# Kernel tuning notes

Hardware: AMD Instinct MI355X
Metric: run time of the kernel (lower is better)

The kernel has to match this reference:

```python
import jax, jax.numpy as jnp
import numpy as np


def setup_inputs() -> dict:
    key = jax.random.key(0)
    k1, k2, k3 = jax.random.split(key, 3)
    B, M, J = 4096, 64, 24  # batch, n_max_markers, n_joints
    points = jax.random.normal(k1, (B, M, 3), dtype=jnp.float32)
    weight = jax.random.uniform(k2, (B, M, J), dtype=jnp.float32)  # positive soft weights
    offset = jax.random.normal(k3, (B, M, J, 3), dtype=jnp.float32)
    return {"points": points, "weight": weight, "offset": offset}


def reference(points, weight, offset):
    # P: per-joint marker offsets (B, J, 3, M); Q: world marker positions (B, 1, 3, M)
    P = jnp.transpose(offset, (0, 2, 3, 1))
    Q = jnp.transpose(points, (0, 2, 1))[:, None]
    w = jnp.transpose(weight, (0, 2, 1))[:, :, None]  # (B, J, 1, M)

    wsum = jnp.sum(w, axis=-1)                   # (B, J, 1)
    P_ = jnp.sum(P * w, axis=-1) / wsum          # (B, J, 3) weighted centroid of offsets
    Q_ = jnp.sum(Q * w, axis=-1) / wsum          # (B, J, 3) weighted centroid of markers

    X = P - P_[..., None]                        # (B, J, 3, M)
    Y = Q - Q_[..., None]                        # (B, J, 3, M) via broadcast

    # Cross-covariance S = X @ Y^T (NOTE: original multiplies un-weighted centered coords)
    S = jnp.einsum('bjdm,bjem->bjde', X, Y)      # (B, J, 3, 3)

    U, _, Vh = jnp.linalg.svd(S)
    V = jnp.swapaxes(Vh, -1, -2)
    Ut = jnp.swapaxes(U, -1, -2)
    det = jnp.linalg.det(jnp.matmul(V, Ut))      # (B, J) reflection correction
    Ut = Ut.at[..., -1, :].multiply(det[..., None])
    R = jnp.matmul(V, Ut)                        # (B, J, 3, 3) optimal rotation
    t = Q_[..., None] - jnp.matmul(R, P_[..., None])  # (B, J, 3, 1)
    return R, t
```

## Files before the change

### kernel.cpp

```cpp
#include <hip/hip_runtime.h>


constexpr int M = 64;
constexpr int J = 24;
constexpr int NACC = 22;
constexpr int NWS  = 15;

constexpr int L4_W = 0;
constexpr int L4_O = 384;
constexpr int L4_P = 1536;
constexpr int L4_N = 1584;

template<int P, int Q>
__device__ __forceinline__ void jrot(float A[4][4], float V[4][4]) {
    float apq = A[P][Q];
    float theta = (A[Q][Q] - A[P][P]) * __builtin_amdgcn_rcpf(2.0f * apq);
    float t = __builtin_amdgcn_rcpf(fabsf(theta) + __builtin_amdgcn_sqrtf(fmaf(theta, theta, 1.0f)));
    t = (theta < 0.0f) ? -t : t;
    t = (apq == 0.0f) ? 0.0f : t;
    float c = __builtin_amdgcn_rsqf(fmaf(t, t, 1.0f));
    float s = t * c;
#pragma unroll
    for (int k = 0; k < 4; ++k) {
        float akp = A[k][P], akq = A[k][Q];
        A[k][P] = c * akp - s * akq;
        A[k][Q] = s * akp + c * akq;
    }
#pragma unroll
    for (int k = 0; k < 4; ++k) {
        float apk = A[P][k], aqk = A[Q][k];
        A[P][k] = c * apk - s * aqk;
        A[Q][k] = s * apk + c * aqk;
        float vkp = V[k][P], vkq = V[k][Q];
        V[k][P] = c * vkp - s * vkq;
        V[k][Q] = s * vkp + c * vkq;
    }
}

__device__ __forceinline__ void horn_solve(
    float S00, float S01, float S02, float S10, float S11, float S12,
    float S20, float S21, float S22,
    float cP0, float cP1, float cP2, float cQ0, float cQ1, float cQ2,
    float* __restrict__ Rout, float* __restrict__ tout)
{
    float A[4][4], V[4][4];
    A[0][0] = S00 + S11 + S22;
    A[0][1] = A[1][0] = S12 - S21;
    A[0][2] = A[2][0] = S20 - S02;
    A[0][3] = A[3][0] = S01 - S10;
    A[1][1] = S00 - S11 - S22;
    A[1][2] = A[2][1] = S01 + S10;
    A[1][3] = A[3][1] = S02 + S20;
    A[2][2] = -S00 + S11 - S22;
    A[2][3] = A[3][2] = S12 + S21;
    A[3][3] = -S00 - S11 + S22;
#pragma unroll
    for (int r = 0; r < 4; ++r)
#pragma unroll
        for (int c = 0; c < 4; ++c)
            V[r][c] = (r == c) ? 1.0f : 0.0f;

#pragma unroll 1
    for (int sweep = 0; sweep < 6; ++sweep) {
        jrot<0, 1>(A, V); jrot<0, 2>(A, V); jrot<0, 3>(A, V);
        jrot<1, 2>(A, V); jrot<1, 3>(A, V); jrot<2, 3>(A, V);
    }

    float best = A[0][0];
    float qw = V[0][0], qx = V[1][0], qy = V[2][0], qz = V[3][0];
#pragma unroll
    for (int i = 1; i < 4; ++i) {
        bool better = A[i][i] > best;
        best = better ? A[i][i] : best;
        qw = better ? V[0][i] : qw;
        qx = better ? V[1][i] : qx;
        qy = better ? V[2][i] : qy;
        qz = better ? V[3][i] : qz;
    }
    float nrm = __builtin_amdgcn_rsqf(qw * qw + qx * qx + qy * qy + qz * qz);
    qw *= nrm; qx *= nrm; qy *= nrm; qz *= nrm;

    float R00 = 1.f - 2.f * (qy * qy + qz * qz);
    float R01 = 2.f * (qx * qy - qw * qz);
    float R02 = 2.f * (qx * qz + qw * qy);
    float R10 = 2.f * (qx * qy + qw * qz);
    float R11 = 1.f - 2.f * (qx * qx + qz * qz);
    float R12 = 2.f * (qy * qz - qw * qx);
    float R20 = 2.f * (qx * qz - qw * qy);
    float R21 = 2.f * (qy * qz + qw * qx);
    float R22 = 1.f - 2.f * (qx * qx + qy * qy);

    Rout[0] = R00; Rout[1] = R01; Rout[2] = R02;
    Rout[3] = R10; Rout[4] = R11; Rout[5] = R12;
    Rout[6] = R20; Rout[7] = R21; Rout[8] = R22;
    tout[0] = cQ0 - (R00 * cP0 + R01 * cP1 + R02 * cP2);
    tout[1] = cQ1 - (R10 * cP0 + R11 * cP1 + R12 * cP2);
    tout[2] = cQ2 - (R20 * cP0 + R21 * cP1 + R22 * cP2);
}

__global__ __launch_bounds__(256, 4) void kabsch_fused(
    const float* __restrict__ points,
    const float* __restrict__ weight,
    const float* __restrict__ offset,
    float* __restrict__ out,
    int bj_total)
{
    const int b = blockIdx.x;
    const int t = threadIdx.x;

    __shared__ float4 lds4[L4_N];

    const float4* wb4 = (const float4*)(weight + (size_t)b * (M * J));
    const float4* ob4 = (const float4*)(offset + (size_t)b * (M * J * 3));
    const float4* pb4 = (const float4*)(points + (size_t)b * (M * 3));

    float4 o0_ = ob4[t];
    float4 o1_ = ob4[t + 256];
    float4 o2_ = ob4[t + 512];
    float4 o3_ = ob4[t + 768];
    float4 w0_ = wb4[t];
    float4 o4_ = {0.f, 0.f, 0.f, 0.f};
    float4 w1_ = {0.f, 0.f, 0.f, 0.f};
    float4 p0_ = {0.f, 0.f, 0.f, 0.f};
    if (t < 128) { o4_ = ob4[1024 + t]; w1_ = wb4[256 + t]; }
    if (t < 48)  { p0_ = pb4[t]; }

    lds4[L4_O + t]        = o0_;
    lds4[L4_O + 256 + t]  = o1_;
    lds4[L4_O + 512 + t]  = o2_;
    lds4[L4_O + 768 + t]  = o3_;
    lds4[L4_W + t]        = w0_;
    if (t < 128) { lds4[L4_O + 1024 + t] = o4_; lds4[L4_W + 256 + t] = w1_; }
    if (t < 48)  { lds4[L4_P + t] = p0_; }

    __syncthreads();

    const int lane = t & 63;
    const int wv   = t >> 6;
    const int kk   = lane & 7;
    const int jj   = (lane >> 3) + wv * 8;
    const bool prod = (jj < J);

    float acc[NACC];
#pragma unroll
    for (int n = 0; n < NACC; ++n) acc[n] = 0.0f;

    if (prod) {
        const float* w_s = (const float*)lds4;
        const float* o_s = (const float*)lds4 + 4 * L4_O;
        const float* p_s = (const float*)lds4 + 4 * L4_P;

#pragma unroll
        for (int i = 0; i < M / 8; ++i) {
            const int m = i * 8 + kk;
            float w  = w_s[m * J + jj];
            float o0 = o_s[m * 72 + jj * 3 + 0];
            float o1 = o_s[m * 72 + jj * 3 + 1];
            float o2 = o_s[m * 72 + jj * 3 + 2];
            float p0 = p_s[m * 3 + 0];
            float p1 = p_s[m * 3 + 1];
            float p2 = p_s[m * 3 + 2];
            acc[0] += w;
            acc[1] = fmaf(w, o0, acc[1]);  acc[2] = fmaf(w, o1, acc[2]);  acc[3] = fmaf(w, o2, acc[3]);
            acc[4] = fmaf(w, p0, acc[4]);  acc[5] = fmaf(w, p1, acc[5]);  acc[6] = fmaf(w, p2, acc[6]);
            acc[7] += o0; acc[8] += o1; acc[9] += o2;
            acc[10] += p0; acc[11] += p1; acc[12] += p2;
            acc[13] = fmaf(o0, p0, acc[13]); acc[14] = fmaf(o0, p1, acc[14]); acc[15] = fmaf(o0, p2, acc[15]);
            acc[16] = fmaf(o1, p0, acc[16]); acc[17] = fmaf(o1, p1, acc[17]); acc[18] = fmaf(o1, p2, acc[18]);
            acc[19] = fmaf(o2, p0, acc[19]); acc[20] = fmaf(o2, p1, acc[20]); acc[21] = fmaf(o2, p2, acc[21]);
        }

#pragma unroll
        for (int n = 0; n < NACC; ++n) {
            float v = acc[n];
            v += __shfl_xor(v, 1);
            v += __shfl_xor(v, 2);
            v += __shfl_xor(v, 4);
            acc[n] = v;
        }
    }

    __syncthreads();

    float* sv_s = (float*)lds4;
    if (prod && kk == 0) {
        const float inv = __builtin_amdgcn_rcpf(acc[0]);
        const float cP0 = acc[1] * inv, cP1 = acc[2] * inv, cP2 = acc[3] * inv;
        const float cQ0 = acc[4] * inv, cQ1 = acc[5] * inv, cQ2 = acc[6] * inv;
        const float To0 = acc[7], To1 = acc[8], To2 = acc[9];
        const float Tp0 = acc[10], Tp1 = acc[11], Tp2 = acc[12];
        const float fM = (float)M;
        float Sv[NWS];
        Sv[0] = acc[13] - cP0 * Tp0 - cQ0 * To0 + fM * cP0 * cQ0;
        Sv[1] = acc[14] - cP0 * Tp1 - cQ1 * To0 + fM * cP0 * cQ1;
        Sv[2] = acc[15] - cP0 * Tp2 - cQ2 * To0 + fM * cP0 * cQ2;
        Sv[3] = acc[16] - cP1 * Tp0 - cQ0 * To1 + fM * cP1 * cQ0;
        Sv[4] = acc[17] - cP1 * Tp1 - cQ1 * To1 + fM * cP1 * cQ1;
        Sv[5] = acc[18] - cP1 * Tp2 - cQ2 * To1 + fM * cP1 * cQ2;
        Sv[6] = acc[19] - cP2 * Tp0 - cQ0 * To2 + fM * cP2 * cQ0;
        Sv[7] = acc[20] - cP2 * Tp1 - cQ1 * To2 + fM * cP2 * cQ1;
        Sv[8] = acc[21] - cP2 * Tp2 - cQ2 * To2 + fM * cP2 * cQ2;
        Sv[9]  = cP0; Sv[10] = cP1; Sv[11] = cP2;
        Sv[12] = cQ0; Sv[13] = cQ1; Sv[14] = cQ2;
#pragma unroll
        for (int n = 0; n < NWS; ++n) sv_s[n * J + jj] = Sv[n];
    }

    __syncthreads();

    if (t < J) {
        float v[NWS];
#pragma unroll
        for (int n = 0; n < NWS; ++n) v[n] = sv_s[n * J + t];
        float Rr[9], tr[3];
        horn_solve(v[0], v[1], v[2], v[3], v[4], v[5], v[6], v[7], v[8],
                   v[9], v[10], v[11], v[12], v[13], v[14], Rr, tr);
        const int bj = b * J + t;
        float* Rout = out + (size_t)bj * 9;
#pragma unroll
        for (int n = 0; n < 9; ++n) Rout[n] = Rr[n];
        float* tout = out + (size_t)bj_total * 9 + (size_t)bj * 3;
        tout[0] = tr[0]; tout[1] = tr[1]; tout[2] = tr[2];
    }
}

extern "C" void kernel_launch(void* const* d_in, const int* in_sizes, int n_in,
                              void* d_out, int out_size, void* d_ws, size_t ws_size,
                              hipStream_t stream) {
    const float* points = (const float*)d_in[0];
    const float* weight = (const float*)d_in[1];
    const float* offset = (const float*)d_in[2];
    float* out = (float*)d_out;

    int B = in_sizes[0] / (M * 3);
    int bj_total = B * J;

    kabsch_fused<<<B, 256, 0, stream>>>(points, weight, offset, out, bj_total);
}
```

Measured before the change: 144.1 us.

## Process four batches per block with register-prefetched global loads

Each block now handles four batch items in sequence. It prefetches the next item's weight, offset and point data into registers while the current item is reduced out of LDS, so global-load latency overlaps with compute. The per-item results are staged in a dedicated LDS array, and a single Horn eigen-solve pass then uses 96 threads instead of 24. In exchange the grid is four times smaller (1024 blocks), which cuts parallelism, and the prefetch raises register pressure.

```diff
diff --git a/kernel.cpp b/kernel.cpp
--- a/kernel.cpp
+++ b/kernel.cpp
@@ -5,6 +5,7 @@
 constexpr int J = 24;
 constexpr int NACC = 22;
 constexpr int NWS  = 15;
+constexpr int BPG  = 4;
 
 constexpr int L4_W = 0;
 constexpr int L4_O = 384;
@@ -103,37 +104,13 @@
     const float* __restrict__ weight,
     const float* __restrict__ offset,
     float* __restrict__ out,
-    int bj_total)
+    int B, int bj_total)
 {
-    const int b = blockIdx.x;
-    const int t = threadIdx.x;
+    const int b0 = blockIdx.x * BPG;
+    const int t  = threadIdx.x;
 
     __shared__ float4 lds4[L4_N];
-
-    const float4* wb4 = (const float4*)(weight + (size_t)b * (M * J));
-    const float4* ob4 = (const float4*)(offset + (size_t)b * (M * J * 3));
-    const float4* pb4 = (const float4*)(points + (size_t)b * (M * 3));
-
-    float4 o0_ = ob4[t];
-    float4 o1_ = ob4[t + 256];
-    float4 o2_ = ob4[t + 512];
-    float4 o3_ = ob4[t + 768];
-    float4 w0_ = wb4[t];
-    float4 o4_ = {0.f, 0.f, 0.f, 0.f};
-    float4 w1_ = {0.f, 0.f, 0.f, 0.f};
-    float4 p0_ = {0.f, 0.f, 0.f, 0.f};
-    if (t < 128) { o4_ = ob4[1024 + t]; w1_ = wb4[256 + t]; }
-    if (t < 48)  { p0_ = pb4[t]; }
-
-    lds4[L4_O + t]        = o0_;
-    lds4[L4_O + 256 + t]  = o1_;
-    lds4[L4_O + 512 + t]  = o2_;
-    lds4[L4_O + 768 + t]  = o3_;
-    lds4[L4_W + t]        = w0_;
-    if (t < 128) { lds4[L4_O + 1024 + t] = o4_; lds4[L4_W + 256 + t] = w1_; }
-    if (t < 48)  { lds4[L4_P + t] = p0_; }
-
-    __syncthreads();
+    __shared__ float  sv_s[BPG][NWS][J + 1];
 
     const int lane = t & 63;
     const int wv   = t >> 6;
@@ -141,86 +118,117 @@
     const int jj   = (lane >> 3) + wv * 8;
     const bool prod = (jj < J);
 
-    float acc[NACC];
-#pragma unroll
-    for (int n = 0; n < NACC; ++n) acc[n] = 0.0f;
-
-    if (prod) {
-        const float* w_s = (const float*)lds4;
-        const float* o_s = (const float*)lds4 + 4 * L4_O;
-        const float* p_s = (const float*)lds4 + 4 * L4_P;
-
-#pragma unroll
-        for (int i = 0; i < M / 8; ++i) {
-            const int m = i * 8 + kk;
-            float w  = w_s[m * J + jj];
-            float o0 = o_s[m * 72 + jj * 3 + 0];
-            float o1 = o_s[m * 72 + jj * 3 + 1];
-            float o2 = o_s[m * 72 + jj * 3 + 2];
-            float p0 = p_s[m * 3 + 0];
-            float p1 = p_s[m * 3 + 1];
-            float p2 = p_s[m * 3 + 2];
-            acc[0] += w;
-            acc[1] = fmaf(w, o0, acc[1]);  acc[2] = fmaf(w, o1, acc[2]);  acc[3] = fmaf(w, o2, acc[3]);
-            acc[4] = fmaf(w, p0, acc[4]);  acc[5] = fmaf(w, p1, acc[5]);  acc[6] = fmaf(w, p2, acc[6]);
-            acc[7] += o0; acc[8] += o1; acc[9] += o2;
-            acc[10] += p0; acc[11] += p1; acc[12] += p2;
-            acc[13] = fmaf(o0, p0, acc[13]); acc[14] = fmaf(o0, p1, acc[14]); acc[15] = fmaf(o0, p2, acc[15]);
-            acc[16] = fmaf(o1, p0, acc[16]); acc[17] = fmaf(o1, p1, acc[17]); acc[18] = fmaf(o1, p2, acc[18]);
-            acc[19] = fmaf(o2, p0, acc[19]); acc[20] = fmaf(o2, p1, acc[20]); acc[21] = fmaf(o2, p2, acc[21]);
+    float4 r_o0, r_o1, r_o2, r_o3, r_o4, r_w0, r_w1, r_p0;
+    auto load_batch = [&](int bb) {
+        bb = bb < B ? bb : B - 1;
+        const float4* wb4 = (const float4*)(weight + (size_t)bb * (M * J));
+        const float4* ob4 = (const float4*)(offset + (size_t)bb * (M * J * 3));
+        const float4* pb4 = (const float4*)(points + (size_t)bb * (M * 3));
+        r_o0 = ob4[t];
+        r_o1 = ob4[t + 256];
+        r_o2 = ob4[t + 512];
+        r_o3 = ob4[t + 768];
+        r_w0 = wb4[t];
+        if (t < 128) { r_o4 = ob4[1024 + t]; r_w1 = wb4[256 + t]; }
+        if (t < 48)  { r_p0 = pb4[t]; }
+    };
+
+    load_batch(b0);
+
+#pragma unroll 1
+    for (int g = 0; g < BPG; ++g) {
+        lds4[L4_O + t]       = r_o0;
+        lds4[L4_O + 256 + t] = r_o1;
+        lds4[L4_O + 512 + t] = r_o2;
+        lds4[L4_O + 768 + t] = r_o3;
+        lds4[L4_W + t]       = r_w0;
+        if (t < 128) { lds4[L4_O + 1024 + t] = r_o4; lds4[L4_W + 256 + t] = r_w1; }
+        if (t < 48)  { lds4[L4_P + t] = r_p0; }
+
+        __syncthreads();
+
+        if (g + 1 < BPG) load_batch(b0 + g + 1);
+
+        float acc[NACC];
+#pragma unroll
+        for (int n = 0; n < NACC; ++n) acc[n] = 0.0f;
+
+        if (prod) {
+            const float* w_s = (const float*)lds4;
+            const float* o_s = (const float*)lds4 + 4 * L4_O;
+            const float* p_s = (const float*)lds4 + 4 * L4_P;
+
+#pragma unroll
+            for (int i = 0; i < M / 8; ++i) {
+                const int m = i * 8 + kk;
+                float w  = w_s[m * J + jj];
+                float o0 = o_s[m * 72 + jj * 3 + 0];
+                float o1 = o_s[m * 72 + jj * 3 + 1];
+                float o2 = o_s[m * 72 + jj * 3 + 2];
+                float p0 = p_s[m * 3 + 0];
+                float p1 = p_s[m * 3 + 1];
+                float p2 = p_s[m * 3 + 2];
+                acc[0] += w;
+                acc[1] = fmaf(w, o0, acc[1]);  acc[2] = fmaf(w, o1, acc[2]);  acc[3] = fmaf(w, o2, acc[3]);
+                acc[4] = fmaf(w, p0, acc[4]);  acc[5] = fmaf(w, p1, acc[5]);  acc[6] = fmaf(w, p2, acc[6]);
+                acc[7] += o0; acc[8] += o1; acc[9] += o2;
+                acc[10] += p0; acc[11] += p1; acc[12] += p2;
+                acc[13] = fmaf(o0, p0, acc[13]); acc[14] = fmaf(o0, p1, acc[14]); acc[15] = fmaf(o0, p2, acc[15]);
+                acc[16] = fmaf(o1, p0, acc[16]); acc[17] = fmaf(o1, p1, acc[17]); acc[18] = fmaf(o1, p2, acc[18]);
+                acc[19] = fmaf(o2, p0, acc[19]); acc[20] = fmaf(o2, p1, acc[20]); acc[21] = fmaf(o2, p2, acc[21]);
+            }
+
+#pragma unroll
+            for (int n = 0; n < NACC; ++n) {
+                float v = acc[n];
+                v += __shfl_xor(v, 1);
+                v += __shfl_xor(v, 2);
+                v += __shfl_xor(v, 4);
+                acc[n] = v;
+            }
+
+            if (kk == 0) {
+                const float inv = __builtin_amdgcn_rcpf(acc[0]);
+                const float cP0 = acc[1] * inv, cP1 = acc[2] * inv, cP2 = acc[3] * inv;
+                const float cQ0 = acc[4] * inv, cQ1 = acc[5] * inv, cQ2 = acc[6] * inv;
+                const float To0 = acc[7], To1 = acc[8], To2 = acc[9];
+                const float Tp0 = acc[10], Tp1 = acc[11], Tp2 = acc[12];
+                const float fM = (float)M;
+                sv_s[g][0][jj]  = acc[13] - cP0 * Tp0 - cQ0 * To0 + fM * cP0 * cQ0;
+                sv_s[g][1][jj]  = acc[14] - cP0 * Tp1 - cQ1 * To0 + fM * cP0 * cQ1;
+                sv_s[g][2][jj]  = acc[15] - cP0 * Tp2 - cQ2 * To0 + fM * cP0 * cQ2;
+                sv_s[g][3][jj]  = acc[16] - cP1 * Tp0 - cQ0 * To1 + fM * cP1 * cQ0;
+                sv_s[g][4][jj]  = acc[17] - cP1 * Tp1 - cQ1 * To1 + fM * cP1 * cQ1;
+                sv_s[g][5][jj]  = acc[18] - cP1 * Tp2 - cQ2 * To1 + fM * cP1 * cQ2;
+                sv_s[g][6][jj]  = acc[19] - cP2 * Tp0 - cQ0 * To2 + fM * cP2 * cQ0;
+                sv_s[g][7][jj]  = acc[20] - cP2 * Tp1 - cQ1 * To2 + fM * cP2 * cQ1;
+                sv_s[g][8][jj]  = acc[21] - cP2 * Tp2 - cQ2 * To2 + fM * cP2 * cQ2;
+                sv_s[g][9][jj]  = cP0; sv_s[g][10][jj] = cP1; sv_s[g][11][jj] = cP2;
+                sv_s[g][12][jj] = cQ0; sv_s[g][13][jj] = cQ1; sv_s[g][14][jj] = cQ2;
+            }
         }
 
-#pragma unroll
-        for (int n = 0; n < NACC; ++n) {
-            float v = acc[n];
-            v += __shfl_xor(v, 1);
-            v += __shfl_xor(v, 2);
-            v += __shfl_xor(v, 4);
-            acc[n] = v;
+        __syncthreads();
+    }
+
+    if (t < BPG * J) {
+        const int g  = t / J;
+        const int j  = t - g * J;
+        const int bb = b0 + g;
+        if (bb < B) {
+            float v[NWS];
+#pragma unroll
+            for (int n = 0; n < NWS; ++n) v[n] = sv_s[g][n][j];
+            float Rr[9], tr[3];
+            horn_solve(v[0], v[1], v[2], v[3], v[4], v[5], v[6], v[7], v[8],
+                       v[9], v[10], v[11], v[12], v[13], v[14], Rr, tr);
+            const int bj = bb * J + j;
+            float* Rout = out + (size_t)bj * 9;
+#pragma unroll
+            for (int n = 0; n < 9; ++n) Rout[n] = Rr[n];
+            float* tout = out + (size_t)bj_total * 9 + (size_t)bj * 3;
+            tout[0] = tr[0]; tout[1] = tr[1]; tout[2] = tr[2];
         }
-    }
-
-    __syncthreads();
-
-    float* sv_s = (float*)lds4;
-    if (prod && kk == 0) {
-        const float inv = __builtin_amdgcn_rcpf(acc[0]);
-        const float cP0 = acc[1] * inv, cP1 = acc[2] * inv, cP2 = acc[3] * inv;
-        const float cQ0 = acc[4] * inv, cQ1 = acc[5] * inv, cQ2 = acc[6] * inv;
-        const float To0 = acc[7], To1 = acc[8], To2 = acc[9];
-        const float Tp0 = acc[10], Tp1 = acc[11], Tp2 = acc[12];
-        const float fM = (float)M;
-        float Sv[NWS];
-        Sv[0] = acc[13] - cP0 * Tp0 - cQ0 * To0 + fM * cP0 * cQ0;
-        Sv[1] = acc[14] - cP0 * Tp1 - cQ1 * To0 + fM * cP0 * cQ1;
-        Sv[2] = acc[15] - cP0 * Tp2 - cQ2 * To0 + fM * cP0 * cQ2;
-        Sv[3] = acc[16] - cP1 * Tp0 - cQ0 * To1 + fM * cP1 * cQ0;
-        Sv[4] = acc[17] - cP1 * Tp1 - cQ1 * To1 + fM * cP1 * cQ1;
-        Sv[5] = acc[18] - cP1 * Tp2 - cQ2 * To1 + fM * cP1 * cQ2;
-        Sv[6] = acc[19] - cP2 * Tp0 - cQ0 * To2 + fM * cP2 * cQ0;
-        Sv[7] = acc[20] - cP2 * Tp1 - cQ1 * To2 + fM * cP2 * cQ1;
-        Sv[8] = acc[21] - cP2 * Tp2 - cQ2 * To2 + fM * cP2 * cQ2;
-        Sv[9]  = cP0; Sv[10] = cP1; Sv[11] = cP2;
-        Sv[12] = cQ0; Sv[13] = cQ1; Sv[14] = cQ2;
-#pragma unroll
-        for (int n = 0; n < NWS; ++n) sv_s[n * J + jj] = Sv[n];
-    }
-
-    __syncthreads();
-
-    if (t < J) {
-        float v[NWS];
-#pragma unroll
-        for (int n = 0; n < NWS; ++n) v[n] = sv_s[n * J + t];
-        float Rr[9], tr[3];
-        horn_solve(v[0], v[1], v[2], v[3], v[4], v[5], v[6], v[7], v[8],
-                   v[9], v[10], v[11], v[12], v[13], v[14], Rr, tr);
-        const int bj = b * J + t;
-        float* Rout = out + (size_t)bj * 9;
-#pragma unroll
-        for (int n = 0; n < 9; ++n) Rout[n] = Rr[n];
-        float* tout = out + (size_t)bj_total * 9 + (size_t)bj * 3;
-        tout[0] = tr[0]; tout[1] = tr[1]; tout[2] = tr[2];
     }
 }
 
@@ -234,6 +242,7 @@
 
     int B = in_sizes[0] / (M * 3);
     int bj_total = B * J;
-
-    kabsch_fused<<<B, 256, 0, stream>>>(points, weight, offset, out, bj_total);
-}
+    int grid = (B + BPG - 1) / BPG;
+
+    kabsch_fused<<<grid, 256, 0, stream>>>(points, weight, offset, out, B, bj_total);
+}
```

Result: no change. 142.5 us (-1.1%).
